# Kernel optimization log

Hardware: AMD Instinct MI355X
Metric: run time of the kernel (lower is better)

## Reference

```python
import jax, jax.numpy as jnp
import numpy as np

HIDDEN = 2048
HEADS = 16
HEAD_DIM = HIDDEN // HEADS
B, L = 4, 2048


def _rotate_half(x):
    x1, x2 = jnp.split(x, 2, axis=-1)
    return jnp.concatenate([-x2, x1], axis=-1)


def setup_inputs() -> dict:
    key = jax.random.key(0)
    k1, k2, k3 = jax.random.split(key, 3)
    x = jax.random.normal(k1, (B, L, HIDDEN), dtype=jnp.float32)
    # realistic rotary tables
    inv_freq = 1.0 / (10000.0 ** (jnp.arange(0, HEAD_DIM, 2, dtype=jnp.float32) / HEAD_DIM))
    t = jnp.arange(L, dtype=jnp.float32)
    freqs = jnp.outer(t, inv_freq)  # [L, HEAD_DIM/2]
    emb = jnp.concatenate([freqs, freqs], axis=-1)  # [L, HEAD_DIM]
    cos = jnp.cos(emb)
    sin = jnp.sin(emb)
    w_qkv = jax.random.normal(k2, (3 * HIDDEN, HIDDEN), dtype=jnp.float32) * (HIDDEN ** -0.5)
    w_out = jax.random.normal(k3, (HIDDEN, HIDDEN), dtype=jnp.float32) * (HIDDEN ** -0.5)
    return {"x": x, "cos": cos, "sin": sin, "w_qkv": w_qkv, "w_out": w_out}


def reference(x, cos, sin, w_qkv, w_out):
    b, l, d = x.shape
    qkv = jnp.einsum('bld,ed->ble', x, w_qkv)  # [B, L, 3D]
    q, k, v = jnp.split(qkv, 3, axis=-1)
    # [B, H, L, Dh]
    q = q.reshape(b, l, HEADS, HEAD_DIM).transpose(0, 2, 1, 3)
    k = k.reshape(b, l, HEADS, HEAD_DIM).transpose(0, 2, 1, 3)
    v = v.reshape(b, l, HEADS, HEAD_DIM).transpose(0, 2, 1, 3)
    cos_ = cos[None, None, :l, :]
    sin_ = sin[None, None, :l, :]
    q = q * cos_ + _rotate_half(q) * sin_
    k = k * cos_ + _rotate_half(k) * sin_
    scale = 1.0 / jnp.sqrt(jnp.asarray(HEAD_DIM, dtype=q.dtype))
    scores = jnp.einsum('bhqd,bhkd->bhqk', q, k) * scale
    attn = jax.nn.softmax(scores, axis=-1)
    out = jnp.einsum('bhqk,bhkd->bhqd', attn, v)  # [B, H, L, Dh]
    out = out.transpose(0, 2, 1, 3).reshape(b, l, d)
    return jnp.einsum('bld,ed->ble', out, w_out)
```

## Files before the change

### kernel.cpp

```cpp
#include <hip/hip_runtime.h>
#include <cstdint>
#include <cstddef>

typedef unsigned short u16;
typedef __attribute__((ext_vector_type(8))) short bf16x8;
typedef __attribute__((ext_vector_type(4))) float f32x4;

#define DEVFN static __device__ __forceinline__

DEVFN u16 f2bf(float f) {
  unsigned u = __float_as_uint(f);
  unsigned r = (u + 0x7FFFu + ((u >> 16) & 1u)) >> 16;
  return (u16)r;
}

DEVFN void gload16(const void* g, void* l) {
  __builtin_amdgcn_global_load_lds(
      (const __attribute__((address_space(1))) void*)g,
      (__attribute__((address_space(3))) void*)l, 16, 0, 0);
}

#define WAITVM(n) asm volatile("s_waitcnt vmcnt(" #n ")" ::: "memory")
#define BARRIER() do { asm volatile("" ::: "memory"); \
                       __builtin_amdgcn_s_barrier();   \
                       asm volatile("" ::: "memory"); } while (0)
#define FENCE_LDS() do { asm volatile("s_waitcnt lgkmcnt(0)" ::: "memory"); \
                         __builtin_amdgcn_sched_barrier(0); } while (0)

__global__ void prep(const float* __restrict__ x, const float* __restrict__ wqkv,
                     const float* __restrict__ wout, const float* __restrict__ cosp,
                     const float* __restrict__ sinp, u16* __restrict__ xb,
                     u16* __restrict__ wqkvb, u16* __restrict__ woutb,
                     float2* __restrict__ cs) {
  constexpr int X4 = 4194304;
  constexpr int W4 = 3145728;
  constexpr int O4 = 1048576;
  int i = blockIdx.x * blockDim.x + threadIdx.x;
  if (i < X4) {
    float4 v = ((const float4*)x)[i];
    unsigned long long w = (unsigned long long)f2bf(v.x)
        | ((unsigned long long)f2bf(v.y) << 16)
        | ((unsigned long long)f2bf(v.z) << 32)
        | ((unsigned long long)f2bf(v.w) << 48);
    *(unsigned long long*)(xb + (size_t)i * 4) = w;
  } else if (i < X4 + W4) {
    int j = i - X4;
    int base = j * 4;
    int e = base >> 11, col = base & 2047;
    int e2;
    if (e < 4096) {
      int part = e >> 11, loc = e & 2047;
      int h = loc >> 7, d = loc & 127;
      int d2 = (d < 64) ? 2 * d : 2 * (d - 64) + 1;
      e2 = part * 2048 + h * 128 + d2;
    } else {
      e2 = e;
    }
    float4 v = *(const float4*)&wqkv[(size_t)base];
    unsigned long long w = (unsigned long long)f2bf(v.x)
        | ((unsigned long long)f2bf(v.y) << 16)
        | ((unsigned long long)f2bf(v.z) << 32)
        | ((unsigned long long)f2bf(v.w) << 48);
    *(unsigned long long*)(wqkvb + (size_t)e2 * 2048 + col) = w;
  } else if (i < X4 + W4 + O4) {
    int j = i - X4 - W4;
    float4 v = ((const float4*)wout)[j];
    unsigned long long w = (unsigned long long)f2bf(v.x)
        | ((unsigned long long)f2bf(v.y) << 16)
        | ((unsigned long long)f2bf(v.z) << 32)
        | ((unsigned long long)f2bf(v.w) << 48);
    *(unsigned long long*)(woutb + (size_t)j * 4) = w;
  } else {
    int k = i - X4 - W4 - O4;
    int ld4 = k * 4;
#pragma unroll
    for (int u = 0; u < 4; u++) {
      int ld = ld4 + u;
      int l = ld >> 6, d = ld & 63;
      cs[ld] = make_float2(cosp[(size_t)l * 128 + d], sinp[(size_t)l * 128 + d]);
    }
  }
}

enum { M_F32OUT = 0, M_ROPE = 1, M_VT = 2 };

DEVFN bf16x8 rdfrag(const u16* buf, int row, int chunk) {
  return *(const bf16x8*)&buf[row * 64 + (((chunk ^ (row & 7)) & 7) << 3)];
}

template <int MODE>
DEVFN void half_mfma0(const u16* Ac, const u16* Bc, int wm, int wn, int quad, int l16,
                      bf16x8 (&bfr)[4][2], f32x4 (&acc)[8][4]) {
#pragma unroll
  for (int j = 0; j < 4; j++)
#pragma unroll
    for (int kk = 0; kk < 2; kk++)
      bfr[j][kk] = rdfrag(Bc, wn * 64 + j * 16 + l16, kk * 4 + quad);
  bf16x8 af[2][2][2];
#pragma unroll
  for (int qi = 0; qi < 2; qi++)
#pragma unroll
    for (int i2 = 0; i2 < 2; i2++)
#pragma unroll
      for (int kk = 0; kk < 2; kk++)
        af[qi][i2][kk] = rdfrag(Ac, wm * 128 + (qi * 2 + i2) * 16 + l16, kk * 4 + quad);
  __builtin_amdgcn_s_setprio(1);
#pragma unroll
  for (int qi = 0; qi < 2; qi++)
#pragma unroll
    for (int kk = 0; kk < 2; kk++)
#pragma unroll
      for (int i2 = 0; i2 < 2; i2++)
#pragma unroll
        for (int j = 0; j < 4; j++) {
          int row = qi * 2 + i2;
          if (MODE == M_VT)
            acc[row][j] = __builtin_amdgcn_mfma_f32_16x16x32_bf16(
                bfr[j][kk], af[qi][i2][kk], acc[row][j], 0, 0, 0);
          else
            acc[row][j] = __builtin_amdgcn_mfma_f32_16x16x32_bf16(
                af[qi][i2][kk], bfr[j][kk], acc[row][j], 0, 0, 0);
        }
  __builtin_amdgcn_s_setprio(0);
}

DEVFN void read_A23(const u16* Ac, int wm, int quad, int l16, bf16x8 (&af)[2][2][2]) {
#pragma unroll
  for (int qi = 0; qi < 2; qi++)
#pragma unroll
    for (int i2 = 0; i2 < 2; i2++)
#pragma unroll
      for (int kk = 0; kk < 2; kk++)
        af[qi][i2][kk] =
            rdfrag(Ac, wm * 128 + ((2 + qi) * 2 + i2) * 16 + l16, kk * 4 + quad);
}

template <int MODE>
DEVFN void mfma23(bf16x8 (&bfr)[4][2], bf16x8 (&af)[2][2][2], f32x4 (&acc)[8][4]) {
  __builtin_amdgcn_s_setprio(1);
#pragma unroll
  for (int qi = 0; qi < 2; qi++)
#pragma unroll
    for (int kk = 0; kk < 2; kk++)
#pragma unroll
      for (int i2 = 0; i2 < 2; i2++)
#pragma unroll
        for (int j = 0; j < 4; j++) {
          int row = (2 + qi) * 2 + i2;
          if (MODE == M_VT)
            acc[row][j] = __builtin_amdgcn_mfma_f32_16x16x32_bf16(
                bfr[j][kk], af[qi][i2][kk], acc[row][j], 0, 0, 0);
          else
            acc[row][j] = __builtin_amdgcn_mfma_f32_16x16x32_bf16(
                af[qi][i2][kk], bfr[j][kk], acc[row][j], 0, 0, 0);
        }
  __builtin_amdgcn_s_setprio(0);
}

template <int MODE>
DEVFN void gemm256_core(const u16* __restrict__ A, const u16* __restrict__ Bt,
                        void* __restrict__ Cv, const float2* __restrict__ cs,
                        int N, int m0, int n0, u16* As, u16* Bs) {
  int tid = threadIdx.x;
  int wv = tid >> 6, lane = tid & 63, quad = lane >> 4, l16 = lane & 15;
  int wm = wv >> 2, wn = wv & 3;

  const u16* pB[2][2];
  const u16* pA[4];
#pragma unroll
  for (int h = 0; h < 2; h++)
#pragma unroll
    for (int o = 0; o < 2; o++) {
      int r = h * 128 + o * 64 + wv * 8 + (lane >> 3);
      int ck = (lane & 7) ^ (r & 7);
      pB[h][o] = Bt + (size_t)(n0 + r) * 2048 + ck * 8;
    }
#pragma unroll
  for (int q = 0; q < 4; q++) {
    int rb = (wv < 4) ? (q * 32 + wv * 8) : (128 + q * 32 + (wv - 4) * 8);
    int r = rb + (lane >> 3);
    int ck = (lane & 7) ^ (r & 7);
    pA[q] = A + (size_t)(m0 + r) * 2048 + ck * 8;
  }

#define STAGE_B(h, buf, kk) do {                                    \
    int rb0_ = (h) * 128 + wv * 8;                                  \
    gload16(pB[h][0] + (kk), &(buf)[rb0_ * 64]);                    \
    gload16(pB[h][1] + (kk), &(buf)[(rb0_ + 64) * 64]); } while (0)
#define STAGE_A(q, buf, kk) do {                                    \
    int rb_ = ((wv < 4) ? ((q) * 32 + wv * 8)                       \
                        : (128 + (q) * 32 + (wv - 4) * 8));         \
    gload16(pA[q] + (kk), &(buf)[rb_ * 64]); } while (0)

  f32x4 acc[8][4] = {};
  bf16x8 bfr[4][2];
  bf16x8 af2[2][2][2];

  STAGE_B(0, Bs, 0);
  STAGE_B(1, Bs, 0);
  STAGE_A(0, As, 0);
  STAGE_A(1, As, 0);
  STAGE_A(2, As, 0);
  STAGE_A(3, As, 0);

  for (int t = 0; t < 31; t++) {
    const u16* Ac = As + (t & 1) * 16384;
    const u16* Bc = Bs + (t & 1) * 16384;
    u16* An = As + ((t + 1) & 1) * 16384;
    u16* Bn = Bs + ((t + 1) & 1) * 16384;
    int kn = (t + 1) * 64;
    STAGE_B(0, Bn, kn);
    STAGE_B(1, Bn, kn);
    WAITVM(4); BARRIER();
    half_mfma0<MODE>(Ac, Bc, wm, wn, quad, l16, bfr, acc);
    read_A23(Ac, wm, quad, l16, af2);
    STAGE_A(0, An, kn);
    STAGE_A(1, An, kn);
    STAGE_A(2, An, kn);
    STAGE_A(3, An, kn);
    BARRIER();
    mfma23<MODE>(bfr, af2, acc);
  }
  {
    const u16* Ac = As + 16384;
    const u16* Bc = Bs + 16384;
    WAITVM(0); BARRIER();
    half_mfma0<MODE>(Ac, Bc, wm, wn, quad, l16, bfr, acc);
    read_A23(Ac, wm, quad, l16, af2);
    mfma23<MODE>(bfr, af2, acc);
  }
#undef STAGE_B
#undef STAGE_A

  if (MODE == M_F32OUT) {
    float* C = (float*)Cv;
#pragma unroll
    for (int i = 0; i < 8; i++)
#pragma unroll
      for (int r = 0; r < 4; r++) {
        size_t row = (size_t)(m0 + wm * 128 + i * 16 + quad * 4 + r);
#pragma unroll
        for (int j = 0; j < 4; j++)
          C[row * N + (n0 + wn * 64 + j * 16 + l16)] = acc[i][j][r];
      }
  } else if (MODE == M_ROPE) {
    constexpr float QSCALE = 1.4426950408889634f * 0.08838834764831845f;
    const float scale = (n0 >> 11) ? 1.0f : QSCALE;
    u16* C = (u16*)Cv;
#pragma unroll
    for (int i = 0; i < 8; i++)
#pragma unroll
      for (int r = 0; r < 4; r++) {
        int row = m0 + wm * 128 + i * 16 + quad * 4 + r;
        int l = row & 2047;
#pragma unroll
        for (int j = 0; j < 4; j++) {
          int col = n0 + wn * 64 + j * 16 + l16;
          int dm = (col & 127) >> 1;
          float2 csv = cs[l * 64 + dm];
          float v = acc[i][j][r];
          float pv = __shfl_xor(v, 1);
          float sg = (l16 & 1) ? csv.y : -csv.y;
          C[(size_t)row * 4096 + col] = f2bf((v * csv.x + pv * sg) * scale);
        }
      }
  } else {
    u16* vt = (u16*)Cv;
#pragma unroll
    for (int j = 0; j < 4; j++)
#pragma unroll
      for (int r = 0; r < 4; r++) {
        int vch = n0 + wn * 64 + j * 16 + quad * 4 + r;
        int h = vch >> 7, d = vch & 127;
#pragma unroll
        for (int i = 0; i < 8; i++) {
          int token = m0 + wm * 128 + i * 16 + l16;
          int b = token >> 11, lloc = token & 2047;
          vt[((size_t)(b * 16 + h)) * 262144 + (size_t)d * 2048 + lloc] =
              f2bf(acc[i][j][r]);
        }
      }
  }
}

__global__ __launch_bounds__(512, 2) void gemm_qkv(const u16* __restrict__ xb,
                                                   const u16* __restrict__ wqkvb,
                                                   u16* __restrict__ qkvo,
                                                   u16* __restrict__ vto,
                                                   const float2* __restrict__ cs) {
  __shared__ u16 As[32768];
  __shared__ u16 Bs[32768];
  int id = blockIdx.x;
  int xcd = id & 7, sub = id >> 3;
  int bx = sub % 24, by = xcd * 4 + sub / 24;
  if (bx < 16)
    gemm256_core<M_ROPE>(xb, wqkvb, qkvo, cs, 0, by * 256, bx * 256, As, Bs);
  else
    gemm256_core<M_VT>(xb, wqkvb + (size_t)4096 * 2048, vto, nullptr, 0,
                       by * 256, (bx - 16) * 256, As, Bs);
}

__global__ __launch_bounds__(512, 2) void gemm_out_k(const u16* __restrict__ A,
                                                     const u16* __restrict__ Bt,
                                                     float* __restrict__ C) {
  __shared__ u16 As[32768];
  __shared__ u16 Bs[32768];
  int id = blockIdx.x;
  int xcd = id & 7, sub = id >> 3;
  int bx = sub % 8, by = xcd * 4 + sub / 8;
  gemm256_core<M_F32OUT>(A, Bt, C, nullptr, 2048, by * 256, bx * 256, As, Bs);
}

DEVFN int swz(int row, int chunk)   { return row * 128 + ((chunk ^ (row & 15)) << 3); }
DEVFN int swz32(int row, int chunk) { return row * 32  + (((chunk ^ (row & 3)) & 3) << 3); }

__global__ __launch_bounds__(256, 3) void attn_fused(const u16* __restrict__ qkv,
                                                     const u16* __restrict__ vt,
                                                     u16* __restrict__ out) {
  __shared__ u16 S[21504];
  u16* const Pb = S + 16384;
  int tid = threadIdx.x;
  int wv = tid >> 6, lane = tid & 63, quad = lane >> 4, l16 = lane & 15;
  int id = blockIdx.x;
  int xcd = id & 7, sub = id >> 3;
  int bh = ((sub >> 4) << 3) | xcd;
  int qt = sub & 15;
  int b = bh >> 4, hh = bh & 15;
  const u16* qptr = qkv + (size_t)b * 2048 * 4096 + hh * 128;
  const u16* kptr = qptr + 2048;
  const u16* vptr = vt + (size_t)bh * 262144;
  int q0 = qt * 128;

#pragma unroll
  for (int j = 0; j < 8; j++) {
    int rb = wv * 4 + j * 16;
    int r = rb + (lane >> 4);
    int ck = (lane & 15) ^ (r & 15);
    gload16(&qptr[(size_t)(q0 + r) * 4096 + ck * 8], &S[rb * 128]);
  }
  __syncthreads();
  bf16x8 qf[2][4];
#pragma unroll
  for (int hf = 0; hf < 2; hf++)
#pragma unroll
    for (int ks = 0; ks < 4; ks++)
      qf[hf][ks] = *(const bf16x8*)&S[swz(wv * 32 + hf * 16 + l16, ks * 4 + quad)];
  __syncthreads();

  f32x4 o[2][8] = {};
  float l[2][4] = {{0.f, 0.f, 0.f, 0.f}, {0.f, 0.f, 0.f, 0.f}};

#pragma unroll
  for (int j = 0; j < 2; j++) {
    int rbk = wv * 4 + j * 16;
    int rk = rbk + (lane >> 4);
    int ckk = (lane & 15) ^ (rk & 15);
    gload16(&kptr[(size_t)rk * 4096 + ckk * 8], &S[rbk * 128]);
    int rbv = wv * 16 + j * 64;
    int rv = rbv + (lane >> 2);
    int ckv = (lane & 3) ^ (rv & 3);
    gload16(&vptr[(size_t)rv * 2048 + ckv * 8], &S[8192 + rbv * 32]);
  }

  for (int kt = 0; kt < 64; kt++) {
    int cur = kt & 1;
    const u16* Kc = S + cur * 4096;
    const u16* Vc = S + 8192 + cur * 4096;
    __syncthreads();
    if (kt < 63) {
      int kk0 = (kt + 1) * 32;
      u16* kb = S + (cur ^ 1) * 4096;
      u16* vb = S + 8192 + (cur ^ 1) * 4096;
#pragma unroll
      for (int j = 0; j < 2; j++) {
        int rbk = wv * 4 + j * 16;
        int rk = rbk + (lane >> 4);
        int ckk = (lane & 15) ^ (rk & 15);
        gload16(&kptr[(size_t)(kk0 + rk) * 4096 + ckk * 8], &kb[rbk * 128]);
        int rbv = wv * 16 + j * 64;
        int rv = rbv + (lane >> 2);
        int ckv = (lane & 3) ^ (rv & 3);
        gload16(&vptr[(size_t)rv * 2048 + kk0 + ckv * 8], &vb[rbv * 32]);
      }
    }
    f32x4 s[2][2] = {};
#pragma unroll
    for (int ks = 0; ks < 4; ks++) {
#pragma unroll
      for (int nt = 0; nt < 2; nt++) {
        bf16x8 bfr = *(const bf16x8*)&Kc[swz(nt * 16 + l16, ks * 4 + quad)];
        s[0][nt] = __builtin_amdgcn_mfma_f32_16x16x32_bf16(qf[0][ks], bfr, s[0][nt], 0, 0, 0);
        s[1][nt] = __builtin_amdgcn_mfma_f32_16x16x32_bf16(qf[1][ks], bfr, s[1][nt], 0, 0, 0);
      }
    }
#pragma unroll
    for (int hf = 0; hf < 2; hf++)
#pragma unroll
      for (int nt = 0; nt < 2; nt++)
#pragma unroll
        for (int r = 0; r < 4; r++) {
          float p = exp2f(s[hf][nt][r]);
          l[hf][r] += p;
          int row = wv * 32 + hf * 16 + quad * 4 + r;
          int col = nt * 16 + l16;
          Pb[row * 40 + col] = f2bf(p);
        }
    FENCE_LDS();
    {
      bf16x8 pf0 = *(const bf16x8*)&Pb[(wv * 32 + l16) * 40 + quad * 8];
      bf16x8 pf1 = *(const bf16x8*)&Pb[(wv * 32 + 16 + l16) * 40 + quad * 8];
#pragma unroll
      for (int nt = 0; nt < 8; nt++) {
        bf16x8 vf = *(const bf16x8*)&Vc[swz32(nt * 16 + l16, quad)];
        o[0][nt] = __builtin_amdgcn_mfma_f32_16x16x32_bf16(pf0, vf, o[0][nt], 0, 0, 0);
        o[1][nt] = __builtin_amdgcn_mfma_f32_16x16x32_bf16(pf1, vf, o[1][nt], 0, 0, 0);
      }
    }
  }
#pragma unroll
  for (int hf = 0; hf < 2; hf++)
#pragma unroll
    for (int r = 0; r < 4; r++)
#pragma unroll
      for (int off = 1; off < 16; off <<= 1) l[hf][r] += __shfl_xor(l[hf][r], off, 16);
  u16* obase = out + ((size_t)b * 2048 + q0) * 2048 + hh * 128;
#pragma unroll
  for (int hf = 0; hf < 2; hf++)
#pragma unroll
    for (int r = 0; r < 4; r++) {
      float inv = 1.0f / l[hf][r];
      int row = wv * 32 + hf * 16 + quad * 4 + r;
#pragma unroll
      for (int nt = 0; nt < 8; nt++)
        obase[(size_t)row * 2048 + nt * 16 + l16] = f2bf(o[hf][nt][r] * inv);
    }
}

extern "C" void kernel_launch(void* const* d_in, const int* in_sizes, int n_in,
                              void* d_out, int out_size, void* d_ws, size_t ws_size,
                              hipStream_t stream) {
  const float* x    = (const float*)d_in[0];
  const float* cosp = (const float*)d_in[1];
  const float* sinp = (const float*)d_in[2];
  const float* wqkv = (const float*)d_in[3];
  const float* wout = (const float*)d_in[4];
  float* outp = (float*)d_out;

  u16* ws    = (u16*)d_ws;
  u16* xb    = ws;
  u16* wqkvb = xb + 16777216;
  u16* woutb = wqkvb + 12582912;
  u16* qkv   = woutb + 4194304;
  u16* vt    = qkv + 33554432;
  float2* cs = (float2*)(vt + 16777216);
  u16* attn  = xb;

  prep<<<32896, 256, 0, stream>>>(x, wqkv, wout, cosp, sinp, xb, wqkvb, woutb, cs);
  gemm_qkv<<<768, 512, 0, stream>>>(xb, wqkvb, qkv, vt, cs);
  attn_fused<<<1024, 256, 0, stream>>>(qkv, vt, attn);
  gemm_out_k<<<256, 512, 0, stream>>>(attn, woutb, outp);
}
```

Before: 571.6 us.

## Transpose QK^T MFMA to pack P stores and remap QKV GEMM block grid

The score MFMA swaps its operands so each lane holds four consecutive key columns of one query row. The four bf16 probabilities can then be written to LDS with one 64-bit store instead of four scalar stores, and the row sum becomes a per-lane scalar reduced with two cross-quad shuffles instead of 16 per-row shuffle chains. Separately, the QKV GEMM block-index mapping changes from bx = sub%24 to bx = sub>>2, which alters which tiles run together on each XCD and so their L2 reuse. The risk is that the new P layout has LDS bank conflicts, and that the remapped grid hurts cache locality.

```diff
diff --git a/kernel.cpp b/kernel.cpp
--- a/kernel.cpp
+++ b/kernel.cpp
@@ -3,6 +3,7 @@
 #include <cstddef>
 
 typedef unsigned short u16;
+typedef unsigned long long u64;
 typedef __attribute__((ext_vector_type(8))) short bf16x8;
 typedef __attribute__((ext_vector_type(4))) float f32x4;
 
@@ -292,7 +293,7 @@
   __shared__ u16 Bs[32768];
   int id = blockIdx.x;
   int xcd = id & 7, sub = id >> 3;
-  int bx = sub % 24, by = xcd * 4 + sub / 24;
+  int bx = sub >> 2, by = xcd * 4 + (sub & 3);
   if (bx < 16)
     gemm256_core<M_ROPE>(xb, wqkvb, qkvo, cs, 0, by * 256, bx * 256, As, Bs);
   else
@@ -348,7 +349,7 @@
   __syncthreads();
 
   f32x4 o[2][8] = {};
-  float l[2][4] = {{0.f, 0.f, 0.f, 0.f}, {0.f, 0.f, 0.f, 0.f}};
+  float lsum[2] = {0.f, 0.f};
 
 #pragma unroll
   for (int j = 0; j < 2; j++) {
@@ -388,23 +389,26 @@
     for (int ks = 0; ks < 4; ks++) {
 #pragma unroll
       for (int nt = 0; nt < 2; nt++) {
-        bf16x8 bfr = *(const bf16x8*)&Kc[swz(nt * 16 + l16, ks * 4 + quad)];
-        s[0][nt] = __builtin_amdgcn_mfma_f32_16x16x32_bf16(qf[0][ks], bfr, s[0][nt], 0, 0, 0);
-        s[1][nt] = __builtin_amdgcn_mfma_f32_16x16x32_bf16(qf[1][ks], bfr, s[1][nt], 0, 0, 0);
-      }
-    }
-#pragma unroll
-    for (int hf = 0; hf < 2; hf++)
-#pragma unroll
-      for (int nt = 0; nt < 2; nt++)
-#pragma unroll
-        for (int r = 0; r < 4; r++) {
-          float p = exp2f(s[hf][nt][r]);
-          l[hf][r] += p;
-          int row = wv * 32 + hf * 16 + quad * 4 + r;
-          int col = nt * 16 + l16;
-          Pb[row * 40 + col] = f2bf(p);
-        }
+        bf16x8 kfr = *(const bf16x8*)&Kc[swz(nt * 16 + l16, ks * 4 + quad)];
+        s[0][nt] = __builtin_amdgcn_mfma_f32_16x16x32_bf16(kfr, qf[0][ks], s[0][nt], 0, 0, 0);
+        s[1][nt] = __builtin_amdgcn_mfma_f32_16x16x32_bf16(kfr, qf[1][ks], s[1][nt], 0, 0, 0);
+      }
+    }
+#pragma unroll
+    for (int hf = 0; hf < 2; hf++) {
+      int row40 = (wv * 32 + hf * 16 + l16) * 40;
+#pragma unroll
+      for (int nt = 0; nt < 2; nt++) {
+        float p0 = exp2f(s[hf][nt][0]);
+        float p1 = exp2f(s[hf][nt][1]);
+        float p2 = exp2f(s[hf][nt][2]);
+        float p3 = exp2f(s[hf][nt][3]);
+        lsum[hf] += (p0 + p1) + (p2 + p3);
+        u64 pk = (u64)f2bf(p0) | ((u64)f2bf(p1) << 16)
+               | ((u64)f2bf(p2) << 32) | ((u64)f2bf(p3) << 48);
+        *(u64*)&Pb[row40 + nt * 16 + quad * 4] = pk;
+      }
+    }
     FENCE_LDS();
     {
       bf16x8 pf0 = *(const bf16x8*)&Pb[(wv * 32 + l16) * 40 + quad * 8];
@@ -418,17 +422,17 @@
     }
   }
 #pragma unroll
+  for (int hf = 0; hf < 2; hf++) {
+    lsum[hf] += __shfl_xor(lsum[hf], 16);
+    lsum[hf] += __shfl_xor(lsum[hf], 32);
+  }
+  u16* obase = out + ((size_t)b * 2048 + q0) * 2048 + hh * 128;
+#pragma unroll
   for (int hf = 0; hf < 2; hf++)
 #pragma unroll
-    for (int r = 0; r < 4; r++)
-#pragma unroll
-      for (int off = 1; off < 16; off <<= 1) l[hf][r] += __shfl_xor(l[hf][r], off, 16);
-  u16* obase = out + ((size_t)b * 2048 + q0) * 2048 + hh * 128;
-#pragma unroll
-  for (int hf = 0; hf < 2; hf++)
-#pragma unroll
     for (int r = 0; r < 4; r++) {
-      float inv = 1.0f / l[hf][r];
+      float lv = __shfl(lsum[hf], quad * 4 + r, 16);
+      float inv = 1.0f / lv;
       int row = wv * 32 + hf * 16 + quad * 4 + r;
 #pragma unroll
       for (int nt = 0; nt < 8; nt++)
```

New measurement: 569.7 us. Within noise of the previous version (-0.3%).
